# Kernel tuning notes

Measured on AMD Instinct MI355X. Metric: run time of the kernel, lower is better.

The kernel has to match this reference:

```python
import jax, jax.numpy as jnp
import numpy as np

B, C, E, K, Hh, Ww = 4, 64, 4, 5, 96, 96


def setup_inputs() -> dict:
    key = jax.random.key(0)
    ks = jax.random.split(key, 18)
    c8 = C // 8
    rn = lambda k, shape, s=0.05: jax.random.normal(k, shape, dtype=jnp.float32) * s
    return {
        "x": rn(ks[0], (B, C, Hh, Ww), 1.0),
        "st_feat": rn(ks[1], (B, C, Hh, Ww), 1.0),
        "kc_w": rn(ks[2], (C * K * K, C)), "kc_b": rn(ks[3], (C * K * K,)),
        "wc": rn(ks[4], (E, c8, C)), "we": rn(ks[5], (E, C, c8)),
        "body1_w": rn(ks[6], (64, 4)), "body1_b": rn(ks[7], (64,)),
        "body2_w": rn(ks[8], (64, 64)), "body2_b": rn(ks[9], (64,)),
        "rout_w": rn(ks[10], (E, 64)), "rout_b": rn(ks[11], (E,)),
        "off_w": rn(ks[12], (2, 64)), "off_b": rn(ks[13], (2,)),
        "stoff_w": rn(ks[14], (2, 64)), "stoff_b": rn(ks[15], (2,)),
        "fus_w": rn(ks[16], (C, 2 * C)), "fus_b": rn(ks[17], (C,)),
        "scale": 2,
    }


def _conv1x1(x, w, b):
    return jnp.einsum('oi,bihw->bohw', w, x) + b[None, :, None, None]


def _sta_conv(feat, kernel, k):
    # spatially-varying depthwise kxk conv: kernel [b, c*k*k, h, w], channel-major (ch*k*k + kh*k + kw)
    b, c, h, w = feat.shape
    pad = (k - 1) // 2
    fp = jnp.pad(feat, ((0, 0), (0, 0), (pad, pad), (pad, pad)), mode='edge')  # replicate pad
    patches = jnp.stack([fp[:, :, i:i + h, j:j + w] for i in range(k) for j in range(k)], axis=2)  # [b,c,k*k,h,w]
    kern = kernel.reshape(b, c, k * k, h, w)
    return jnp.sum(patches * kern, axis=2)


def _grid_sample(img, offset, sh, sw, H, W):
    # bilinear, zero padding, align_corners=True; offset [1or b, 2, H, W] in source-pixel units
    b, c, h, w = img.shape
    gx = ((jnp.arange(W, dtype=jnp.float32) + 0.5) / sw - 0.5) * 2.0 / (w - 1) - 1.0
    gy = ((jnp.arange(H, dtype=jnp.float32) + 0.5) / sh - 0.5) * 2.0 / (h - 1) - 1.0
    gx = jnp.broadcast_to(gx[None, None, :] + offset[:, 0] * 2.0 / (w - 1), (b, H, W))
    gy = jnp.broadcast_to(gy[None, :, None] + offset[:, 1] * 2.0 / (h - 1), (b, H, W))
    px = (gx + 1.0) * 0.5 * (w - 1)
    py = (gy + 1.0) * 0.5 * (h - 1)
    x0 = jnp.floor(px)
    y0 = jnp.floor(py)
    imgf = img.reshape(b, c, h * w)

    def gather(ix, iy):
        valid = (ix >= 0) & (ix <= w - 1) & (iy >= 0) & (iy <= h - 1)
        ixc = jnp.clip(ix, 0, w - 1).astype(jnp.int32)
        iyc = jnp.clip(iy, 0, h - 1).astype(jnp.int32)
        idx = (iyc * w + ixc).reshape(b, 1, H * W)
        v = jnp.take_along_axis(imgf, idx, axis=2).reshape(b, c, H, W)
        return v * valid.astype(img.dtype)[:, None]

    wx1 = (px - x0)[:, None]
    wy1 = (py - y0)[:, None]
    wx0 = 1.0 - wx1
    wy0 = 1.0 - wy1
    return (wy0 * wx0 * gather(x0, y0) + wy0 * wx1 * gather(x0 + 1.0, y0)
            + wy1 * wx0 * gather(x0, y0 + 1.0) + wy1 * wx1 * gather(x0 + 1.0, y0 + 1.0))


def _forward(x, st_feat, kc_w, kc_b, wc, we, body1_w, body1_b, body2_w, body2_b,
             rout_w, rout_b, off_w, off_b, stoff_w, stoff_b, fus_w, fus_b, scale):
    b, c, h, w = x.shape
    sh = sw = float(scale)
    H, W = int(h * sh), int(w * sw)
    c8 = c // 8
    num_e = wc.shape[0]

    kernel_warp = jax.nn.leaky_relu(_conv1x1(st_feat, kc_w, kc_b), 0.1)  # [b, c*K*K, h, w]
    sta_feat = _sta_conv(x, kernel_warp, K)

    # coordinate embedding input [1, 4, H, W]
    ch = (jnp.arange(H, dtype=jnp.float32) + 0.5) / sh
    coor_h = ch - jnp.floor(ch + 0.001) - 0.5  # [H]
    cw = (jnp.arange(W, dtype=jnp.float32) + 0.5) / sw
    coor_w = cw - jnp.floor(cw + 0.001) - 0.5  # [W]
    ones = jnp.ones((H, W), dtype=jnp.float32)
    inp = jnp.stack([ones / sw, ones / sh,
                     jnp.broadcast_to(coor_h[:, None], (H, W)),
                     jnp.broadcast_to(coor_w[None, :], (H, W))], axis=0)[None]

    emb = jax.nn.relu(_conv1x1(jax.nn.relu(_conv1x1(inp, body1_w, body1_b)), body2_w, body2_b))
    offset = _conv1x1(emb, off_w, off_b)       # [1, 2, H, W]
    st_offset = _conv1x1(emb, stoff_w, stoff_b)
    routing = jax.nn.sigmoid(_conv1x1(emb, rout_w, rout_b))  # [1, E, H, W]

    r = routing[0].reshape(num_e, H * W).T  # [HW, E]
    wc_px = (r @ wc.reshape(num_e, -1)).reshape(H, W, c8, c)
    we_px = (r @ we.reshape(num_e, -1)).reshape(H, W, c, c8)

    fea0 = _grid_sample(x, offset, sh, sw, H, W)  # [b, c, H, W]
    t = jnp.einsum('hwoc,bchw->bhwo', wc_px, fea0)
    fea = jnp.einsum('hwco,bhwo->bchw', we_px, t) + fea0

    sta_hr = _grid_sample(sta_feat, st_offset, sh, sw, H, W)
    out = _conv1x1(jnp.concatenate([sta_hr, fea], axis=1), fus_w, fus_b)
    return out


def reference(x, st_feat, kc_w, kc_b, wc, we, body1_w, body1_b, body2_w, body2_b,
              rout_w, rout_b, off_w, off_b, stoff_w, stoff_b, fus_w, fus_b, scale):
    return _forward(x, st_feat, kc_w, kc_b, wc, we, body1_w, body1_b, body2_w, body2_b,
                    rout_w, rout_b, off_w, off_b, stoff_w, stoff_b, fus_w, fus_b, scale)
```

## Files before the change

### kernel.cpp

```cpp
#include <hip/hip_runtime.h>

typedef __attribute__((ext_vector_type(8))) _Float16 h8;
typedef __attribute__((ext_vector_type(4))) _Float16 h4;
typedef __attribute__((ext_vector_type(4))) float f32x4;

__device__ __forceinline__ _Float16 f2h(float f) { return (_Float16)f; }
__device__ __forceinline__ float h2f(_Float16 h) { return (float)h; }

__device__ __forceinline__ int fswz(int p, int i) { return p * 128 + (i ^ ((p & 7) << 3)); }

#define WS_STA   0u
#define WS_GSI   4718592u
#define WS_GSF   4718656u
#define WS_WCPX  4718720u
#define WS_WEPX  4726912u
#define WS_FUSB  4735104u
#define WS_KCB   4751488u
#define WS_KCW   4757888u

__global__ __launch_bounds__(256) void k_prep(
    const float* __restrict__ kc_w, const float* __restrict__ kc_b,
    const float* __restrict__ fusw,
    _Float16* __restrict__ kcw, _Float16* __restrict__ fusB,
    float* __restrict__ kcbp)
{
  int e = blockIdx.x * 256 + threadIdx.x;
  if (e < 25600) {
    int jp = e >> 4, i0 = (e & 15) << 2;
    int w = jp / 400, rem = jp % 400;
    int t = rem >> 4, cl = rem & 15;
    int j = (w * 16 + cl) * 25 + t;
    const float4* src = (const float4*)(kc_w + j * 64 + i0);
    float4 v = *src;
    h4 ov;
    ov[0] = f2h(v.x); ov[1] = f2h(v.y); ov[2] = f2h(v.z); ov[3] = f2h(v.w);
    *(h4*)(kcw + jp * 64 + i0) = ov;
  }
  if (e < 8192) {
    int Nt = e >> 11, ks = (e >> 9) & 3, l = (e >> 3) & 63, j = e & 7;
    fusB[e] = f2h(fusw[(Nt * 16 + (l & 15)) * 128 + (l >> 4) * 8 + 32 * ks + j]);
  }
  if (e < 1600) {
    int w = e / 400, rem = e % 400, t = rem >> 4, cl = rem & 15;
    kcbp[e] = kc_b[(w * 16 + cl) * 25 + t];
  }
}

__global__ __launch_bounds__(256) void k_embed(
    const float* __restrict__ b1w, const float* __restrict__ b1b,
    const float* __restrict__ b2w, const float* __restrict__ b2b,
    const float* __restrict__ rw,  const float* __restrict__ rb,
    const float* __restrict__ ow,  const float* __restrict__ ob,
    const float* __restrict__ sow, const float* __restrict__ sob,
    const float* __restrict__ wc,  const float* __restrict__ we,
    int* __restrict__ gs_i, float* __restrict__ gs_f,
    float* __restrict__ wcpx, float* __restrict__ wepx)
{
  __shared__ float l_w2[4096];
  __shared__ float l_h1[4][64];
  __shared__ float l_h2[4][64];
  __shared__ float l_sm[4][8];
  int tid = threadIdx.x;
  for (int e = tid; e < 4096; e += 256) l_w2[e] = b2w[e];
  int g = tid >> 6, o = tid & 63;
  float py = (g >> 1) ? 1.f : 0.f;
  float pxx = (g & 1) ? 1.f : 0.f;
  float chh = (py + 0.5f) * 0.5f;
  float coh = chh - floorf(chh + 0.001f) - 0.5f;
  float cww = (pxx + 0.5f) * 0.5f;
  float cow = cww - floorf(cww + 0.001f) - 0.5f;
  float z = b1b[o] + b1w[o * 4 + 0] * 0.5f + b1w[o * 4 + 1] * 0.5f
          + b1w[o * 4 + 2] * coh + b1w[o * 4 + 3] * cow;
  l_h1[g][o] = fmaxf(z, 0.f);
  __syncthreads();
  float z2 = b2b[o];
  #pragma unroll 8
  for (int i = 0; i < 64; i++) z2 = fmaf(l_w2[o * 64 + i], l_h1[g][i], z2);
  l_h2[g][o] = fmaxf(z2, 0.f);
  __syncthreads();
  if (o < 8) {
    const float* wp; float bias;
    if (o < 4)      { wp = rw  + o * 64;       bias = rb[o]; }
    else if (o < 6) { wp = ow  + (o - 4) * 64; bias = ob[o - 4]; }
    else            { wp = sow + (o - 6) * 64; bias = sob[o - 6]; }
    float acc = bias;
    for (int i = 0; i < 64; i++) acc = fmaf(wp[i], l_h2[g][i], acc);
    if (o < 4) acc = 1.f / (1.f + expf(-acc));
    l_sm[g][o] = acc;
  }
  __syncthreads();
  if (o == 0) {
    float qbx = (g & 1) ? 0.25f : -0.25f;
    float qby = (g >> 1) ? 0.25f : -0.25f;
    float qx  = qbx + l_sm[g][4]; float fx  = floorf(qx);
    float qy  = qby + l_sm[g][5]; float fy  = floorf(qy);
    float qsx = qbx + l_sm[g][6]; float fsx = floorf(qsx);
    float qsy = qby + l_sm[g][7]; float fsy = floorf(qsy);
    gs_i[g * 4 + 0] = (int)fx;  gs_f[g * 4 + 0] = qx - fx;
    gs_i[g * 4 + 1] = (int)fy;  gs_f[g * 4 + 1] = qy - fy;
    gs_i[g * 4 + 2] = (int)fsx; gs_f[g * 4 + 2] = qsx - fsx;
    gs_i[g * 4 + 3] = (int)fsy; gs_f[g * 4 + 3] = qsy - fsy;
  }
  float r0 = l_sm[g][0], r1 = l_sm[g][1], r2 = l_sm[g][2], r3 = l_sm[g][3];
  for (int idx = o; idx < 512; idx += 64) {
    wcpx[g * 512 + idx] = r0 * wc[idx] + r1 * wc[512 + idx] + r2 * wc[1024 + idx] + r3 * wc[1536 + idx];
    wepx[g * 512 + idx] = r0 * we[idx] + r1 * we[512 + idx] + r2 * we[1024 + idx] + r3 * we[1536 + idx];
  }
}

__global__ __launch_bounds__(256, 4) void k_sta(
    const float* __restrict__ x, const float* __restrict__ st,
    const _Float16* __restrict__ kcw, const float* __restrict__ kcbp,
    _Float16* __restrict__ sta_out)
{
  __shared__ __align__(16) _Float16 x_lds[64 * 5 * 40];
  __shared__ __align__(16) _Float16 st_lds[32 * 72];
  int wg = (blockIdx.x & 7) * 144 + (blockIdx.x >> 3);
  int b = wg / 288;
  int r1 = wg % 288;
  int hb = r1 / 3, wb = r1 % 3;
  int tid = threadIdx.x, lane = tid & 63, w = tid >> 6;
  for (int e = tid; e < 2560; e += 256) {
    int row = e >> 3, v = e & 7;
    int rr = row % 5;
    int grow = min(max(hb + rr - 2, 0), 95);
    float4 val = *(const float4*)&x[((b * 64 + (row / 5)) * 96 + grow) * 96 + 32 * wb + v * 4];
    _Float16* dst = &x_lds[row * 40 + 2 + v * 4];
    dst[0] = f2h(val.x); dst[1] = f2h(val.y); dst[2] = f2h(val.z); dst[3] = f2h(val.w);
  }
  for (int e = tid; e < 1280; e += 256) {
    int row = e >> 2, j = e & 3;
    int col = (j < 2) ? j : 32 + j;
    int rr = row % 5;
    int grow = min(max(hb + rr - 2, 0), 95);
    int gcol = min(max(32 * wb + col - 2, 0), 95);
    x_lds[row * 40 + col] = f2h(x[((b * 64 + (row / 5)) * 96 + grow) * 96 + gcol]);
  }
  for (int e = tid; e < 512; e += 256) {
    int c = e >> 3, p0 = (e & 7) * 4;
    float4 v = *(const float4*)&st[((size_t)(b * 64 + c) * 96 + hb) * 96 + 32 * wb + p0];
    st_lds[(p0 + 0) * 72 + c] = f2h(v.x);
    st_lds[(p0 + 1) * 72 + c] = f2h(v.y);
    st_lds[(p0 + 2) * 72 + c] = f2h(v.z);
    st_lds[(p0 + 3) * 72 + c] = f2h(v.w);
  }
  __syncthreads();
  int l15 = lane & 15, lg = lane >> 4;
  h8 afrag[2][2];
  #pragma unroll
  for (int ms = 0; ms < 2; ms++)
    #pragma unroll
    for (int ks = 0; ks < 2; ks++)
      afrag[ms][ks] = *(const h8*)&st_lds[(ms * 16 + l15) * 72 + 32 * ks + lg * 8];
  float sta_acc[2][4];
  #pragma unroll
  for (int ms = 0; ms < 2; ms++)
    #pragma unroll
    for (int r = 0; r < 4; r++) sta_acc[ms][r] = 0.f;
  for (int dh = 0; dh < 5; dh++) {
    h4 xa[2][2];
    #pragma unroll
    for (int ms = 0; ms < 2; ms++) {
      const _Float16* xp = &x_lds[((w * 16 + l15) * 5 + dh) * 40 + ms * 16 + lg * 4];
      xa[ms][0] = *(const h4*)xp;
      xa[ms][1] = *(const h4*)(xp + 4);
    }
    #pragma unroll
    for (int dw = 0; dw < 5; dw++) {
      int jbase = w * 400 + (dh * 5 + dw) * 16;
      const _Float16* bp = kcw + (jbase + l15) * 64 + lg * 8;
      h8 bf0 = *(const h8*)bp;
      h8 bf1 = *(const h8*)(bp + 32);
      float kb = kcbp[jbase + l15];
      #pragma unroll
      for (int ms = 0; ms < 2; ms++) {
        f32x4 acc = {0.f, 0.f, 0.f, 0.f};
        acc = __builtin_amdgcn_mfma_f32_16x16x32_f16(afrag[ms][0], bf0, acc, 0, 0, 0);
        acc = __builtin_amdgcn_mfma_f32_16x16x32_f16(afrag[ms][1], bf1, acc, 0, 0, 0);
        #pragma unroll
        for (int r = 0; r < 4; r++) {
          float kw = acc[r] + kb;
          kw = (kw >= 0.f) ? kw : 0.1f * kw;
          int ci = r + dw;
          float xvf = h2f(ci < 4 ? xa[ms][0][ci] : xa[ms][1][ci - 4]);
          sta_acc[ms][r] = fmaf(kw, xvf, sta_acc[ms][r]);
        }
      }
    }
  }
  {
    _Float16* lds2 = &x_lds[w * 3200];
    #pragma unroll
    for (int ms = 0; ms < 2; ms++) {
      h4 ov;
      #pragma unroll
      for (int r = 0; r < 4; r++) ov[r] = f2h(sta_acc[ms][r]);
      *(h4*)&lds2[l15 * 36 + ms * 16 + lg * 4] = ov;
    }
    int ch = lane >> 2, q = lane & 3;
    h4 lo = *(const h4*)&lds2[ch * 36 + q * 8];
    h4 hi = *(const h4*)&lds2[ch * 36 + q * 8 + 4];
    h8 ov;
    #pragma unroll
    for (int r = 0; r < 4; r++) { ov[r] = lo[r]; ov[r + 4] = hi[r]; }
    *(h8*)(sta_out + ((size_t)(b * 64 + w * 16 + ch) * 96 + hb) * 96 + 32 * wb + q * 8) = ov;
  }
}

__global__ __launch_bounds__(256) void k_main(
    const float* __restrict__ x, const _Float16* __restrict__ sta,
    const int* __restrict__ gs_i, const float* __restrict__ gs_f,
    const float* __restrict__ wcpx, const float* __restrict__ wepx,
    const _Float16* __restrict__ fusB, const float* __restrict__ fusb,
    float* __restrict__ out)
{
  __shared__ __align__(16) _Float16 feat[64 * 128];
  __shared__ float t_lds[8][68];
  int wg = (blockIdx.x & 7) * 288 + (blockIdx.x >> 3);
  int b = wg / 576, r = wg % 576;
  int y = r / 3, xb = r % 3;
  int tid = threadIdx.x, px = tid & 63, fg = tid >> 6;
  int xg = xb * 64 + px;
  int v = ((y & 1) << 1) | (xg & 1);
  int idxo = gs_i[v * 4 + 0], idyo = gs_i[v * 4 + 1], idxs = gs_i[v * 4 + 2], idys = gs_i[v * 4 + 3];
  float wx1 = gs_f[v * 4 + 0], wy1 = gs_f[v * 4 + 1], sx1 = gs_f[v * 4 + 2], sy1 = gs_f[v * 4 + 3];
  int xh = xg >> 1, yh = y >> 1;
  int ix0 = xh + idxo, iy0 = yh + idyo;
  float wx0 = 1.f - wx1, wy0 = 1.f - wy1;
  bool vx0 = (unsigned)ix0 < 96u, vx1 = (unsigned)(ix0 + 1) < 96u;
  bool vy0 = (unsigned)iy0 < 96u, vy1 = (unsigned)(iy0 + 1) < 96u;
  int cx0 = min(max(ix0, 0), 95), cx1 = min(max(ix0 + 1, 0), 95);
  int cy0 = min(max(iy0, 0), 95), cy1 = min(max(iy0 + 1, 0), 95);
  float ww00 = (vx0 && vy0) ? wy0 * wx0 : 0.f;
  float ww10 = (vx1 && vy0) ? wy0 * wx1 : 0.f;
  float ww01 = (vx0 && vy1) ? wy1 * wx0 : 0.f;
  float ww11 = (vx1 && vy1) ? wy1 * wx1 : 0.f;
  int a00 = cy0 * 96 + cx0, a10 = cy0 * 96 + cx1, a01 = cy1 * 96 + cx0, a11 = cy1 * 96 + cx1;
  int jx0 = xh + idxs, jy0 = yh + idys;
  float sx0 = 1.f - sx1, sy0 = 1.f - sy1;
  bool ux0 = (unsigned)jx0 < 96u, ux1 = (unsigned)(jx0 + 1) < 96u;
  bool uy0 = (unsigned)jy0 < 96u, uy1 = (unsigned)(jy0 + 1) < 96u;
  int dx0 = min(max(jx0, 0), 95), dx1 = min(max(jx0 + 1, 0), 95);
  int dy0 = min(max(jy0, 0), 95), dy1 = min(max(jy0 + 1, 0), 95);
  float sw00 = (ux0 && uy0) ? sy0 * sx0 : 0.f;
  float sw10 = (ux1 && uy0) ? sy0 * sx1 : 0.f;
  float sw01 = (ux0 && uy1) ? sy1 * sx0 : 0.f;
  float sw11 = (ux1 && uy1) ? sy1 * sx1 : 0.f;
  int s00 = dy0 * 96 + dx0, s10 = dy0 * 96 + dx1, s01 = dy1 * 96 + dx0, s11 = dy1 * 96 + dx1;
  h8 stv0, stv1, fev0, fev1;
  #pragma unroll
  for (int k = 0; k < 16; k++) {
    int ch = fg * 16 + k;
    const float* xc = x + (size_t)(b * 64 + ch) * 9216;
    float f0 = ww00 * xc[a00] + ww10 * xc[a10] + ww01 * xc[a01] + ww11 * xc[a11];
    const _Float16* sc = sta + (size_t)(b * 64 + ch) * 9216;
    float s0 = sw00 * h2f(sc[s00]) + sw10 * h2f(sc[s10]) + sw01 * h2f(sc[s01]) + sw11 * h2f(sc[s11]);
    if (k < 8) { stv0[k] = f2h(s0); fev0[k] = f2h(f0); }
    else       { stv1[k - 8] = f2h(s0); fev1[k - 8] = f2h(f0); }
  }
  *(h8*)&feat[fswz(px, fg * 16)]          = stv0;
  *(h8*)&feat[fswz(px, fg * 16 + 8)]      = stv1;
  *(h8*)&feat[fswz(px, 64 + fg * 16)]     = fev0;
  *(h8*)&feat[fswz(px, 64 + fg * 16 + 8)] = fev1;
  __syncthreads();
  {
    int o2 = fg * 2;
    int v0 = (y & 1) << 1;
    int base = __builtin_amdgcn_readfirstlane((v0 * 8 + o2) * 64);
    const float* w00 = wcpx + base;
    const float* w01 = wcpx + base + 64;
    const float* w10 = wcpx + base + 512;
    const float* w11 = wcpx + base + 512 + 64;
    float acc00 = 0.f, acc01 = 0.f, acc10 = 0.f, acc11 = 0.f;
    #pragma unroll
    for (int cb = 0; cb < 8; cb++) {
      h8 blk = *(const h8*)&feat[fswz(px, 64 + cb * 8)];
      #pragma unroll
      for (int q = 0; q < 8; q++) {
        float fv = h2f(blk[q]);
        int c = cb * 8 + q;
        acc00 = fmaf(w00[c], fv, acc00);
        acc01 = fmaf(w01[c], fv, acc01);
        acc10 = fmaf(w10[c], fv, acc10);
        acc11 = fmaf(w11[c], fv, acc11);
      }
    }
    bool odd = (xg & 1);
    t_lds[o2][px]     = odd ? acc10 : acc00;
    t_lds[o2 + 1][px] = odd ? acc11 : acc01;
  }
  __syncthreads();
  {
    float tv[8];
    #pragma unroll
    for (int oo = 0; oo < 8; oo++) tv[oo] = t_lds[oo][px];
    int v0 = (y & 1) << 1;
    bool odd = (xg & 1);
    int wbase = __builtin_amdgcn_readfirstlane((v0 * 64 + fg * 16) * 8);
    #pragma unroll
    for (int blki = 0; blki < 2; blki++) {
      h8 f0b = *(const h8*)&feat[fswz(px, 64 + fg * 16 + blki * 8)];
      h8 ob2;
      #pragma unroll
      for (int q = 0; q < 8; q++) {
        int k = blki * 8 + q;
        const float* wA = wepx + wbase + k * 8;
        const float* wB = wA + 512;
        float sA = 0.f, sB = 0.f;
        #pragma unroll
        for (int oo = 0; oo < 8; oo++) { sA = fmaf(wA[oo], tv[oo], sA); sB = fmaf(wB[oo], tv[oo], sB); }
        float fe = h2f(f0b[q]) + (odd ? sB : sA);
        ob2[q] = f2h(fe);
      }
      *(h8*)&feat[fswz(px, 64 + fg * 16 + blki * 8)] = ob2;
    }
  }
  __syncthreads();
  {
    int l15 = px & 15, lg = px >> 4;
    h8 af[4];
    #pragma unroll
    for (int ks = 0; ks < 4; ks++)
      af[ks] = *(const h8*)&feat[fswz(fg * 16 + l15, lg * 8 + 32 * ks)];
    #pragma unroll
    for (int Nt = 0; Nt < 4; Nt++) {
      f32x4 acc = {0.f, 0.f, 0.f, 0.f};
      #pragma unroll
      for (int ks = 0; ks < 4; ks++) {
        h8 bfv = *(const h8*)&fusB[((Nt * 4 + ks) * 64 + px) * 8];
        acc = __builtin_amdgcn_mfma_f32_16x16x32_f16(af[ks], bfv, acc, 0, 0, 0);
      }
      int c = Nt * 16 + l15;
      float bias = fusb[c];
      float4 o4;
      o4.x = acc[0] + bias; o4.y = acc[1] + bias; o4.z = acc[2] + bias; o4.w = acc[3] + bias;
      float* op = out + ((size_t)(b * 64 + c) * 192 + y) * 192 + xb * 64 + fg * 16 + lg * 4;
      *(float4*)op = o4;
    }
  }
}

extern "C" void kernel_launch(void* const* d_in, const int* in_sizes, int n_in,
                              void* d_out, int out_size, void* d_ws, size_t ws_size,
                              hipStream_t stream)
{
  (void)in_sizes; (void)n_in; (void)out_size; (void)ws_size;
  const float* x    = (const float*)d_in[0];
  const float* st   = (const float*)d_in[1];
  const float* kc_w = (const float*)d_in[2];
  const float* kc_b = (const float*)d_in[3];
  const float* wc   = (const float*)d_in[4];
  const float* we   = (const float*)d_in[5];
  const float* b1w  = (const float*)d_in[6];
  const float* b1b  = (const float*)d_in[7];
  const float* b2w  = (const float*)d_in[8];
  const float* b2b  = (const float*)d_in[9];
  const float* rw   = (const float*)d_in[10];
  const float* rb   = (const float*)d_in[11];
  const float* ow   = (const float*)d_in[12];
  const float* ob   = (const float*)d_in[13];
  const float* sow  = (const float*)d_in[14];
  const float* sob  = (const float*)d_in[15];
  const float* fusw = (const float*)d_in[16];
  const float* fusb = (const float*)d_in[17];
  char* ws = (char*)d_ws;
  _Float16* sta  = (_Float16*)(ws + WS_STA);
  int*   gsi  = (int*)(ws + WS_GSI);
  float* gsf  = (float*)(ws + WS_GSF);
  float* wcpxp = (float*)(ws + WS_WCPX);
  float* wepxp = (float*)(ws + WS_WEPX);
  _Float16* fusB = (_Float16*)(ws + WS_FUSB);
  float* kcbp = (float*)(ws + WS_KCB);
  _Float16* kcw = (_Float16*)(ws + WS_KCW);
  float* outp = (float*)d_out;

  k_prep<<<dim3(100), dim3(256), 0, stream>>>(kc_w, kc_b, fusw, kcw, fusB, kcbp);
  k_embed<<<dim3(1), dim3(256), 0, stream>>>(b1w, b1b, b2w, b2b, rw, rb, ow, ob,
                                             sow, sob, wc, we, gsi, gsf, wcpxp, wepxp);
  k_sta<<<dim3(1152), dim3(256), 0, stream>>>(x, st, kcw, kcbp, sta);
  k_main<<<dim3(2304), dim3(256), 0, stream>>>(x, sta, gsi, gsf, wcpxp, wepxp, fusB, fusb, outp);
}
```

Baseline: 200.2 us.

## Split k_sta M-subtiles across 512 threads and tile the sta intermediate layout

k_sta now launches 512 threads per block. Each half of the block handles one of the two 16-pixel M-subtiles, where one thread used to loop over both, which halves per-thread registers and the serial MFMA chain. The sta intermediate is stored in a tiled layout ([b][row][32-col block][channel][32]). This lets each thread write its h4 directly, removing the LDS transpose step, and k_main's sta gather addressing is updated to match. The risks are more threads sharing the same LDS budget and different locality for k_main's bilinear gathers from sta.

```diff
diff --git a/kernel.cpp b/kernel.cpp
--- a/kernel.cpp
+++ b/kernel.cpp
@@ -108,7 +108,7 @@
   }
 }
 
-__global__ __launch_bounds__(256, 4) void k_sta(
+__global__ __launch_bounds__(512, 8) void k_sta(
     const float* __restrict__ x, const float* __restrict__ st,
     const _Float16* __restrict__ kcw, const float* __restrict__ kcbp,
     _Float16* __restrict__ sta_out)
@@ -119,8 +119,9 @@
   int b = wg / 288;
   int r1 = wg % 288;
   int hb = r1 / 3, wb = r1 % 3;
-  int tid = threadIdx.x, lane = tid & 63, w = tid >> 6;
-  for (int e = tid; e < 2560; e += 256) {
+  int tid = threadIdx.x, lane = tid & 63;
+  int w = (tid >> 6) & 3, half = tid >> 8;
+  for (int e = tid; e < 2560; e += 512) {
     int row = e >> 3, v = e & 7;
     int rr = row % 5;
     int grow = min(max(hb + rr - 2, 0), 95);
@@ -128,7 +129,7 @@
     _Float16* dst = &x_lds[row * 40 + 2 + v * 4];
     dst[0] = f2h(val.x); dst[1] = f2h(val.y); dst[2] = f2h(val.z); dst[3] = f2h(val.w);
   }
-  for (int e = tid; e < 1280; e += 256) {
+  for (int e = tid; e < 1280; e += 512) {
     int row = e >> 2, j = e & 3;
     int col = (j < 2) ? j : 32 + j;
     int rr = row % 5;
@@ -136,7 +137,7 @@
     int gcol = min(max(32 * wb + col - 2, 0), 95);
     x_lds[row * 40 + col] = f2h(x[((b * 64 + (row / 5)) * 96 + grow) * 96 + gcol]);
   }
-  for (int e = tid; e < 512; e += 256) {
+  for (int e = tid; e < 512; e += 512) {
     int c = e >> 3, p0 = (e & 7) * 4;
     float4 v = *(const float4*)&st[((size_t)(b * 64 + c) * 96 + hb) * 96 + 32 * wb + p0];
     st_lds[(p0 + 0) * 72 + c] = f2h(v.x);
@@ -146,25 +147,17 @@
   }
   __syncthreads();
   int l15 = lane & 15, lg = lane >> 4;
-  h8 afrag[2][2];
+  h8 afrag[2];
   #pragma unroll
-  for (int ms = 0; ms < 2; ms++)
-    #pragma unroll
-    for (int ks = 0; ks < 2; ks++)
-      afrag[ms][ks] = *(const h8*)&st_lds[(ms * 16 + l15) * 72 + 32 * ks + lg * 8];
-  float sta_acc[2][4];
+  for (int ks = 0; ks < 2; ks++)
+    afrag[ks] = *(const h8*)&st_lds[(half * 16 + l15) * 72 + 32 * ks + lg * 8];
+  float sta_acc[4];
   #pragma unroll
-  for (int ms = 0; ms < 2; ms++)
-    #pragma unroll
-    for (int r = 0; r < 4; r++) sta_acc[ms][r] = 0.f;
+  for (int r = 0; r < 4; r++) sta_acc[r] = 0.f;
   for (int dh = 0; dh < 5; dh++) {
-    h4 xa[2][2];
-    #pragma unroll
-    for (int ms = 0; ms < 2; ms++) {
-      const _Float16* xp = &x_lds[((w * 16 + l15) * 5 + dh) * 40 + ms * 16 + lg * 4];
-      xa[ms][0] = *(const h4*)xp;
-      xa[ms][1] = *(const h4*)(xp + 4);
-    }
+    const _Float16* xp = &x_lds[((w * 16 + l15) * 5 + dh) * 40 + half * 16 + lg * 4];
+    h4 xa0 = *(const h4*)xp;
+    h4 xa1 = *(const h4*)(xp + 4);
     #pragma unroll
     for (int dw = 0; dw < 5; dw++) {
       int jbase = w * 400 + (dh * 5 + dw) * 16;
@@ -172,38 +165,25 @@
       h8 bf0 = *(const h8*)bp;
       h8 bf1 = *(const h8*)(bp + 32);
       float kb = kcbp[jbase + l15];
+      f32x4 acc = {0.f, 0.f, 0.f, 0.f};
+      acc = __builtin_amdgcn_mfma_f32_16x16x32_f16(afrag[0], bf0, acc, 0, 0, 0);
+      acc = __builtin_amdgcn_mfma_f32_16x16x32_f16(afrag[1], bf1, acc, 0, 0, 0);
       #pragma unroll
-      for (int ms = 0; ms < 2; ms++) {
-        f32x4 acc = {0.f, 0.f, 0.f, 0.f};
-        acc = __builtin_amdgcn_mfma_f32_16x16x32_f16(afrag[ms][0], bf0, acc, 0, 0, 0);
-        acc = __builtin_amdgcn_mfma_f32_16x16x32_f16(afrag[ms][1], bf1, acc, 0, 0, 0);
-        #pragma unroll
-        for (int r = 0; r < 4; r++) {
-          float kw = acc[r] + kb;
-          kw = (kw >= 0.f) ? kw : 0.1f * kw;
-          int ci = r + dw;
-          float xvf = h2f(ci < 4 ? xa[ms][0][ci] : xa[ms][1][ci - 4]);
-          sta_acc[ms][r] = fmaf(kw, xvf, sta_acc[ms][r]);
-        }
+      for (int r = 0; r < 4; r++) {
+        float kw = acc[r] + kb;
+        kw = (kw >= 0.f) ? kw : 0.1f * kw;
+        int ci = r + dw;
+        float xvf = h2f(ci < 4 ? xa0[ci] : xa1[ci - 4]);
+        sta_acc[r] = fmaf(kw, xvf, sta_acc[r]);
       }
     }
   }
   {
-    _Float16* lds2 = &x_lds[w * 3200];
-    #pragma unroll
-    for (int ms = 0; ms < 2; ms++) {
-      h4 ov;
-      #pragma unroll
-      for (int r = 0; r < 4; r++) ov[r] = f2h(sta_acc[ms][r]);
-      *(h4*)&lds2[l15 * 36 + ms * 16 + lg * 4] = ov;
-    }
-    int ch = lane >> 2, q = lane & 3;
-    h4 lo = *(const h4*)&lds2[ch * 36 + q * 8];
-    h4 hi = *(const h4*)&lds2[ch * 36 + q * 8 + 4];
-    h8 ov;
-    #pragma unroll
-    for (int r = 0; r < 4; r++) { ov[r] = lo[r]; ov[r + 4] = hi[r]; }
-    *(h8*)(sta_out + ((size_t)(b * 64 + w * 16 + ch) * 96 + hb) * 96 + 32 * wb + q * 8) = ov;
+    h4 ov;
+    #pragma unroll
+    for (int r = 0; r < 4; r++) ov[r] = f2h(sta_acc[r]);
+    _Float16* tp = sta_out + ((size_t)((b * 96 + hb) * 3 + wb) << 11);
+    *(h4*)(tp + (w * 16 + l15) * 32 + half * 16 + lg * 4) = ov;
   }
 }
 
@@ -246,14 +226,17 @@
   float sw10 = (ux1 && uy0) ? sy0 * sx1 : 0.f;
   float sw01 = (ux0 && uy1) ? sy1 * sx0 : 0.f;
   float sw11 = (ux1 && uy1) ? sy1 * sx1 : 0.f;
-  int s00 = dy0 * 96 + dx0, s10 = dy0 * 96 + dx1, s01 = dy1 * 96 + dx0, s11 = dy1 * 96 + dx1;
+  int s00 = (((b * 96 + dy0) * 3 + (dx0 >> 5)) << 11) + (dx0 & 31);
+  int s10 = (((b * 96 + dy0) * 3 + (dx1 >> 5)) << 11) + (dx1 & 31);
+  int s01 = (((b * 96 + dy1) * 3 + (dx0 >> 5)) << 11) + (dx0 & 31);
+  int s11 = (((b * 96 + dy1) * 3 + (dx1 >> 5)) << 11) + (dx1 & 31);
   h8 stv0, stv1, fev0, fev1;
   #pragma unroll
   for (int k = 0; k < 16; k++) {
     int ch = fg * 16 + k;
     const float* xc = x + (size_t)(b * 64 + ch) * 9216;
     float f0 = ww00 * xc[a00] + ww10 * xc[a10] + ww01 * xc[a01] + ww11 * xc[a11];
-    const _Float16* sc = sta + (size_t)(b * 64 + ch) * 9216;
+    const _Float16* sc = sta + ch * 32;
     float s0 = sw00 * h2f(sc[s00]) + sw10 * h2f(sc[s10]) + sw01 * h2f(sc[s01]) + sw11 * h2f(sc[s11]);
     if (k < 8) { stv0[k] = f2h(s0); fev0[k] = f2h(f0); }
     else       { stv1[k - 8] = f2h(s0); fev1[k - 8] = f2h(f0); }
@@ -377,6 +360,6 @@
   k_prep<<<dim3(100), dim3(256), 0, stream>>>(kc_w, kc_b, fusw, kcw, fusB, kcbp);
   k_embed<<<dim3(1), dim3(256), 0, stream>>>(b1w, b1b, b2w, b2b, rw, rb, ow, ob,
                                              sow, sob, wc, we, gsi, gsf, wcpxp, wepxp);
-  k_sta<<<dim3(1152), dim3(256), 0, stream>>>(x, st, kcw, kcbp, sta);
+  k_sta<<<dim3(1152), dim3(512), 0, stream>>>(x, st, kcw, kcbp, sta);
   k_main<<<dim3(2304), dim3(256), 0, stream>>>(x, sta, gsi, gsf, wcpxp, wepxp, fusB, fusb, outp);
 }
```

Result: slower. 268.1 us (+33.9%).
